# Kernel optimization log

Measured on AMD Instinct MI355X. Metric: run time of the kernel, lower is better.

## Reference

```python
import jax, jax.numpy as jnp
import numpy as np
import math

B, T, D_MODEL, N_HEAD = 2, 2048, 1024, 16
NUM_BUCKETS, MAX_DIST = 32, 128
D_HEAD = D_MODEL // N_HEAD


def _relative_position_bucket(rel_pos, num_buckets=NUM_BUCKETS, max_distance=MAX_DIST):
    # bidirectional=True branch of the torch code
    nb = num_buckets // 2
    buckets = (rel_pos > 0).astype(jnp.int32) * nb
    rel_pos = jnp.abs(rel_pos)
    max_exact = nb // 2
    is_small = rel_pos < max_exact
    # guard log(0); masked out by is_small anyway
    large = max_exact + (
        jnp.log(jnp.maximum(rel_pos, 1).astype(jnp.float32) / max_exact)
        / math.log(max_distance / max_exact) * (nb - max_exact)
    ).astype(jnp.int32)
    large = jnp.minimum(large, nb - 1)
    return buckets + jnp.where(is_small, rel_pos, large)


def compute_bias(rel_bias, q_len, kv_len):
    qp = jnp.arange(q_len, dtype=jnp.int32)[:, None]
    kp = jnp.arange(kv_len, dtype=jnp.int32)[None, :]
    buckets = _relative_position_bucket(kp - qp)          # [Tq, Tkv]
    vals = rel_bias[buckets]                              # [Tq, Tkv, H]
    return jnp.transpose(vals, (2, 0, 1))                 # [H, Tq, Tkv]


def setup_inputs() -> dict:
    key = jax.random.key(0)
    ks = jax.random.split(key, 9)
    inp = {
        'q': jax.random.normal(ks[0], (B, T, D_MODEL), jnp.float32),
        'k': jax.random.normal(ks[1], (B, T, D_MODEL), jnp.float32),
        'v': jax.random.normal(ks[2], (B, T, D_MODEL), jnp.float32),
        'mask': jax.random.randint(ks[3], (B, T, T), 0, 2, jnp.int32),
        'Wq': jax.random.normal(ks[4], (D_MODEL, D_MODEL), jnp.float32) * 0.02,
        'Wk': jax.random.normal(ks[5], (D_MODEL, D_MODEL), jnp.float32) * 0.02,
        'Wv': jax.random.normal(ks[6], (D_MODEL, D_MODEL), jnp.float32) * 0.02,
        'Wfc': jax.random.normal(ks[7], (D_MODEL, D_MODEL), jnp.float32) * 0.02,
        'rel_bias': jax.random.normal(ks[8], (NUM_BUCKETS, N_HEAD), jnp.float32) * 0.02,
    }
    return inp


def reference(q, k, v, mask, Wq, Wk, Wv, Wfc, rel_bias):
    b, tq, _ = q.shape
    tkv = k.shape[1]
    qh = (q @ Wq).reshape(b, tq, N_HEAD, D_HEAD)
    kh = (k @ Wk).reshape(b, tkv, N_HEAD, D_HEAD)
    vh = (v @ Wv).reshape(b, tkv, N_HEAD, D_HEAD)
    attn = jnp.einsum('blhd,bthd->bhlt', qh, kh) / np.sqrt(D_HEAD).astype(np.float32)
    position_bias = compute_bias(rel_bias, tq, tkv)       # [H, Tq, Tkv]
    attn = attn + position_bias[None]                     # broadcast over batch
    attn = jnp.where(mask[:, None] == 0, -1e9, attn)
    attn = jax.nn.softmax(attn, axis=-1)                  # dropout: eval mode (identity)
    out = jnp.einsum('bhlt,bthd->blhd', attn, vh).reshape(b, tq, D_MODEL)
    out = out @ Wfc
    return out, position_bias[:, None]                    # bias returned as [H,1,Tq,Tkv] like torch
```

## Files before the change

kernel.cpp:

```cpp
#include <hip/hip_runtime.h>
#include <math.h>

#define TT 2048
#define BB 2
#define HH 16
#define DMODEL 1024
#define NREL 4095

typedef __attribute__((ext_vector_type(8)))  _Float16 half8;
typedef __attribute__((ext_vector_type(4)))  _Float16 half4;
typedef __attribute__((ext_vector_type(16))) float    f32x16;
typedef __attribute__((ext_vector_type(4)))  int      int4v;

#define EXP2F(x) __builtin_amdgcn_exp2f(x)

__device__ __forceinline__ f32x16 zero16() {
    f32x16 v;
#pragma unroll
    for (int i = 0; i < 16; ++i) v[i] = 0.f;
    return v;
}

__device__ __forceinline__ unsigned pkh(float a, float b) {
    union { _Float16 h[2]; unsigned u; } x;
    x.h[0] = (_Float16)a; x.h[1] = (_Float16)b;
    return x.u;
}

__device__ __forceinline__ void gload16(const void* g, void* l) {
    __builtin_amdgcn_global_load_lds(
        (const __attribute__((address_space(1))) void*)g,
        (__attribute__((address_space(3))) void*)l, 16, 0, 0);
}

__device__ __forceinline__ int rel_bucket(int rel) {
    int base = rel > 0 ? 16 : 0;
    int r = rel < 0 ? -rel : rel;
    int lb;
    if (r < 8)       lb = r;
    else if (r < 12) lb = 8;
    else if (r < 16) lb = 9;
    else if (r < 23) lb = 10;
    else if (r < 32) lb = 11;
    else if (r < 46) lb = 12;
    else if (r < 64) lb = 13;
    else if (r < 91) lb = 14;
    else             lb = 15;
    return base + lb;
}

__global__ __launch_bounds__(256) void prep_kernel(
    const int* __restrict__ mask,
    const float* __restrict__ W0, const float* __restrict__ W1,
    const float* __restrict__ W2, const float* __restrict__ W3,
    const float* __restrict__ rel_bias,
    _Float16* __restrict__ WT,
    float* __restrict__ btable, unsigned* __restrict__ mb)
{
    __shared__ float t[64][65];
    int bid = blockIdx.x, tid = threadIdx.x;
    if (bid < 256) {
        int idx = bid * 256 + tid;
        if (idx < HH * NREL) {
            int h = idx / NREL, ri = idx % NREL;
            btable[idx] = rel_bias[rel_bucket(ri - (TT - 1)) * HH + h];
        }
    } else if (bid < 1280) {
        int zz = (bid - 256) >> 8, inner = (bid - 256) & 255;
        const float* src = zz == 0 ? W0 : zz == 1 ? W1 : zz == 2 ? W2 : W3;
        _Float16* dst = WT + (size_t)zz * DMODEL * DMODEL;
        int k0 = (inner >> 4) * 64, n0 = (inner & 15) * 64;
        int r = tid >> 4, c4 = (tid & 15) * 4;
#pragma unroll
        for (int i = 0; i < 4; ++i) {
            float4 vv = *(const float4*)(src + (size_t)(k0 + r + 16 * i) * DMODEL + n0 + c4);
            t[r + 16 * i][c4] = vv.x; t[r + 16 * i][c4 + 1] = vv.y;
            t[r + 16 * i][c4 + 2] = vv.z; t[r + 16 * i][c4 + 3] = vv.w;
        }
        __syncthreads();
        int rn = tid >> 2, ck = (tid & 3) * 16;
        half8 h0, h1;
#pragma unroll
        for (int j = 0; j < 8; ++j) h0[j] = (_Float16)t[ck + j][rn];
#pragma unroll
        for (int j = 0; j < 8; ++j) h1[j] = (_Float16)t[ck + 8 + j][rn];
        *(half8*)(dst + (size_t)(n0 + rn) * DMODEL + k0 + ck) = h0;
        *(half8*)(dst + (size_t)(n0 + rn) * DMODEL + k0 + ck + 8) = h1;
    } else {
        int g = (bid - 1280) * 256 + tid;
        int vv = mask[g];
        unsigned long long bal = __ballot(vv != 0);
        if ((g & 63) == 0) {
            int word = g >> 5;
            mb[word]     = (unsigned)bal;
            mb[word + 1] = (unsigned)(bal >> 32);
        }
    }
}

__global__ __launch_bounds__(256) void gemm_proj3(
    const float* __restrict__ qf32, const float* __restrict__ kf32,
    const float* __restrict__ vf32, const _Float16* __restrict__ WT,
    _Float16* __restrict__ qhf, _Float16* __restrict__ khf,
    _Float16* __restrict__ vtf, int zbase)
{
    __shared__ __align__(16) char lds[65536];
    int z = zbase + blockIdx.z;
    const float* A = z == 0 ? qf32 : z == 1 ? kf32 : vf32;
    const _Float16* Bt = WT + (size_t)z * DMODEL * DMODEL;
    int bm = blockIdx.x * 128, bn = blockIdx.y * 128;
    int tid = threadIdx.x;
    int wv = tid >> 6, lane = tid & 63, hi = lane >> 5;
    int lo = lane & 31;
    int wr = wv >> 1, wc = wv & 1;
    int srow = wv * 32 + (lane >> 3);
    int scol = (lane & 7) * 8;
    const float*    Abase = A  + (size_t)(bm + srow) * DMODEL + scol;
    const _Float16* Bbase = Bt + (size_t)(bn + srow) * DMODEL + scol;
    int awoff = wv * 4096 + (lane >> 3) * 128 + (lane & 7) * 16;

    f32x16 acc[2][2];
    acc[0][0] = zero16(); acc[0][1] = zero16();
    acc[1][0] = zero16(); acc[1][1] = zero16();

    float4 ra[8];
    auto loadA = [&](int kt) {
#pragma unroll
        for (int t = 0; t < 4; ++t) {
            ra[2 * t]     = *(const float4*)(Abase + (size_t)t * 8 * DMODEL + kt * 64);
            ra[2 * t + 1] = *(const float4*)(Abase + (size_t)t * 8 * DMODEL + kt * 64 + 4);
        }
    };
    auto gloadB = [&](int buf, int kt) {
#pragma unroll
        for (int t = 0; t < 4; ++t)
            gload16(Bbase + (size_t)t * 8 * DMODEL + kt * 64, lds + buf + 16384 + wv * 4096 + t * 1024);
    };
    auto writeA = [&](int buf) {
#pragma unroll
        for (int t = 0; t < 4; ++t) {
            float4 v0 = ra[2 * t], v1 = ra[2 * t + 1];
            half8 h = {(_Float16)v0.x, (_Float16)v0.y, (_Float16)v0.z, (_Float16)v0.w,
                       (_Float16)v1.x, (_Float16)v1.y, (_Float16)v1.z, (_Float16)v1.w};
            *(half8*)(lds + buf + awoff + t * 1024) = h;
        }
    };
    auto compute = [&](int buf) {
#pragma unroll
        for (int kk = 0; kk < 4; ++kk) {
            int cs = 2 * kk + hi;
            half8 a[2], b[2];
#pragma unroll
            for (int i = 0; i < 2; ++i) {
                a[i] = *(const half8*)(lds + buf + (wr * 64 + i * 32 + lo) * 128 + cs * 16);
                b[i] = *(const half8*)(lds + buf + 16384 + (wc * 64 + i * 32 + lo) * 128 + cs * 16);
            }
            acc[0][0] = __builtin_amdgcn_mfma_f32_32x32x16_f16(a[0], b[0], acc[0][0], 0, 0, 0);
            acc[0][1] = __builtin_amdgcn_mfma_f32_32x32x16_f16(a[0], b[1], acc[0][1], 0, 0, 0);
            acc[1][0] = __builtin_amdgcn_mfma_f32_32x32x16_f16(a[1], b[0], acc[1][0], 0, 0, 0);
            acc[1][1] = __builtin_amdgcn_mfma_f32_32x32x16_f16(a[1], b[1], acc[1][1], 0, 0, 0);
        }
    };

    loadA(0); gloadB(0, 0); writeA(0);
    __syncthreads();
    for (int kt = 0; kt < 16; kt += 2) {
        loadA(kt + 1); gloadB(32768, kt + 1);
        compute(0);
        writeA(32768);
        __syncthreads();
        if (kt + 2 < 16) { loadA(kt + 2); gloadB(0, kt + 2); }
        compute(32768);
        if (kt + 2 < 16) writeA(0);
        __syncthreads();
    }

    if (z < 2) {
        _Float16* C = z == 0 ? qhf : khf;
#pragma unroll
        for (int j = 0; j < 2; ++j) {
            int n = bn + wc * 64 + j * 32 + lo;
            int h = n >> 6, d = n & 63;
#pragma unroll
            for (int i = 0; i < 2; ++i) {
                int mb2 = bm + wr * 64 + i * 32 + 4 * hi;
#pragma unroll
                for (int r = 0; r < 16; ++r) {
                    int m = mb2 + (r & 3) + 8 * (r >> 2);
                    int b = m >> 11, t = m & (TT - 1);
                    C[((size_t)(b * HH + h) * TT + t) * 64 + d] = (_Float16)acc[i][j][r];
                }
            }
        }
    } else {
#pragma unroll
        for (int j = 0; j < 2; ++j) {
            int n = bn + wc * 64 + j * 32 + lo;
            int h = n >> 6, d = n & 63;
#pragma unroll
            for (int i = 0; i < 2; ++i) {
                int mb2 = bm + wr * 64 + i * 32 + 4 * hi;
                int b = mb2 >> 11, tb = mb2 & (TT - 1);
#pragma unroll
                for (int r4 = 0; r4 < 4; ++r4) {
                    half4 hv = {(_Float16)acc[i][j][4 * r4 + 0], (_Float16)acc[i][j][4 * r4 + 1],
                                (_Float16)acc[i][j][4 * r4 + 2], (_Float16)acc[i][j][4 * r4 + 3]};
                    *(half4*)(vtf + ((size_t)(b * HH + h) * 64 + d) * TT + tb + 8 * r4) = hv;
                }
            }
        }
    }
}

__global__ __launch_bounds__(256) void attn_mfma(
    const _Float16* __restrict__ qh, const _Float16* __restrict__ kh,
    const _Float16* __restrict__ vt, const unsigned* __restrict__ maskbits,
    const float* __restrict__ btable, _Float16* __restrict__ Oout)
{
    __shared__ float bias_lds[4096];
    int bid = blockIdx.x;
    int xcd = bid & 7, j = bid >> 3;
    int qt = j & 15, bh = xcd + 8 * (j >> 4);
    int h = bh & 15, b = bh >> 4;
    int tid = threadIdx.x;
    int wv = tid >> 6, lane = tid & 63, lo = lane & 31, hi = lane >> 5;
    int q0 = qt * 128 + wv * 32;

    {
        const float* bsrc = btable + h * NREL;
#pragma unroll
        for (int i = 0; i < 16; ++i) {
            int idx = i * 256 + tid;
            bias_lds[idx] = bsrc[idx < NREL ? idx : NREL - 1] * 1.44269504f;
        }
    }

    const size_t bhoff = (size_t)(b * HH + h);
    const _Float16* Q = qh + (bhoff * TT + q0) * 64;
    const _Float16* K = kh + bhoff * TT * 64;
    const _Float16* V = vt + bhoff * 64 * TT;

    half8 qf[4];
#pragma unroll
    for (int c = 0; c < 4; ++c)
        qf[c] = *(const half8*)(Q + (size_t)lo * 64 + c * 16 + hi * 8);

    const int bofs = (TT - 1) - (q0 + lo) + 4 * hi;
    const unsigned* mw = maskbits + ((size_t)b * TT + q0 + lo) * 64;
    const float SC = 0.125f * 1.44269504f;

    f32x16 acco0 = zero16(), acco1 = zero16();
    float m = -INFINITY, l = 0.f;

    __syncthreads();

    for (int kt = 0; kt < 16; ++kt) {
        int k0 = kt * 128;
        unsigned wmA0 = mw[4 * kt], wmA1 = mw[4 * kt + 1];
        unsigned wmB0 = mw[4 * kt + 2], wmB1 = mw[4 * kt + 3];

        f32x16 sA0 = zero16(), sA1 = zero16(), sB0 = zero16(), sB1 = zero16();
        {
            half8 kf[4];
#pragma unroll
            for (int c = 0; c < 4; ++c)
                kf[c] = *(const half8*)(K + (size_t)(k0 + lo) * 64 + c * 16 + hi * 8);
            __builtin_amdgcn_s_setprio(1);
#pragma unroll
            for (int c = 0; c < 4; ++c)
                sA0 = __builtin_amdgcn_mfma_f32_32x32x16_f16(kf[c], qf[c], sA0, 0, 0, 0);
            __builtin_amdgcn_s_setprio(0);
#pragma unroll
            for (int c = 0; c < 4; ++c)
                kf[c] = *(const half8*)(K + (size_t)(k0 + 32 + lo) * 64 + c * 16 + hi * 8);
            __builtin_amdgcn_s_setprio(1);
#pragma unroll
            for (int c = 0; c < 4; ++c)
                sA1 = __builtin_amdgcn_mfma_f32_32x32x16_f16(kf[c], qf[c], sA1, 0, 0, 0);
            __builtin_amdgcn_s_setprio(0);
#pragma unroll
            for (int c = 0; c < 4; ++c)
                kf[c] = *(const half8*)(K + (size_t)(k0 + 64 + lo) * 64 + c * 16 + hi * 8);
            __builtin_amdgcn_s_setprio(1);
#pragma unroll
            for (int c = 0; c < 4; ++c)
                sB0 = __builtin_amdgcn_mfma_f32_32x32x16_f16(kf[c], qf[c], sB0, 0, 0, 0);
            __builtin_amdgcn_s_setprio(0);
#pragma unroll
            for (int c = 0; c < 4; ++c)
                kf[c] = *(const half8*)(K + (size_t)(k0 + 96 + lo) * 64 + c * 16 + hi * 8);
            __builtin_amdgcn_s_setprio(1);
#pragma unroll
            for (int c = 0; c < 4; ++c)
                sB1 = __builtin_amdgcn_mfma_f32_32x32x16_f16(kf[c], qf[c], sB1, 0, 0, 0);
            __builtin_amdgcn_s_setprio(0);
        }

        unsigned wsA0 = wmA0 >> (hi * 4), wsA1 = wmA1 >> (hi * 4);
        unsigned wsB0 = wmB0 >> (hi * 4), wsB1 = wmB1 >> (hi * 4);
        int bbase = bofs + k0;
#pragma unroll
        for (int r = 0; r < 16; ++r) {
            int sh = (r & 3) + 8 * (r >> 2);
            float a0 = fmaf(sA0[r], SC, bias_lds[bbase + sh]);
            float a1 = fmaf(sA1[r], SC, bias_lds[bbase + sh + 32]);
            float b0 = fmaf(sB0[r], SC, bias_lds[bbase + sh + 64]);
            float b1 = fmaf(sB1[r], SC, bias_lds[bbase + sh + 96]);
            sA0[r] = ((wsA0 >> sh) & 1) ? a0 : -1e9f;
            sA1[r] = ((wsA1 >> sh) & 1) ? a1 : -1e9f;
            sB0[r] = ((wsB0 >> sh) & 1) ? b0 : -1e9f;
            sB1[r] = ((wsB1 >> sh) & 1) ? b1 : -1e9f;
        }

        float tr[8];
#pragma unroll
        for (int r = 0; r < 8; ++r) {
            float x0 = fmaxf(fmaxf(sA0[r], sA0[r + 8]), fmaxf(sA1[r], sA1[r + 8]));
            float x1 = fmaxf(fmaxf(sB0[r], sB0[r + 8]), fmaxf(sB1[r], sB1[r + 8]));
            tr[r] = fmaxf(x0, x1);
        }
#pragma unroll
        for (int r = 0; r < 4; ++r) tr[r] = fmaxf(tr[r], tr[r + 4]);
        float tm = fmaxf(fmaxf(tr[0], tr[1]), fmaxf(tr[2], tr[3]));
        tm = fmaxf(tm, __shfl_xor(tm, 32));
        float mnew = fmaxf(m, tm);
        float corr = EXP2F(m - mnew);
        m = mnew;

#pragma unroll
        for (int r = 0; r < 16; ++r) sA0[r] = EXP2F(sA0[r] - m);
#pragma unroll
        for (int r = 0; r < 16; ++r) sA1[r] = EXP2F(sA1[r] - m);
#pragma unroll
        for (int r = 0; r < 16; ++r) sB0[r] = EXP2F(sB0[r] - m);
#pragma unroll
        for (int r = 0; r < 16; ++r) sB1[r] = EXP2F(sB1[r] - m);
#pragma unroll
        for (int r = 0; r < 8; ++r)
            tr[r] = ((sA0[r] + sA0[r + 8]) + (sA1[r] + sA1[r + 8]))
                  + ((sB0[r] + sB0[r + 8]) + (sB1[r] + sB1[r + 8]));
#pragma unroll
        for (int r = 0; r < 4; ++r) tr[r] += tr[r + 4];
        float rs = (tr[0] + tr[1]) + (tr[2] + tr[3]);
        rs += __shfl_xor(rs, 32);
        l = l * corr + rs;
#pragma unroll
        for (int r = 0; r < 16; ++r) { acco0[r] *= corr; acco1[r] *= corr; }

        half8 pbA[4], pbB[4];
#pragma unroll
        for (int g = 0; g < 2; ++g)
#pragma unroll
            for (int hc = 0; hc < 2; ++hc) {
                int r0 = hc * 8;
                float p0 = g ? sA1[r0 + 0] : sA0[r0 + 0];
                float p1 = g ? sA1[r0 + 1] : sA0[r0 + 1];
                float p2 = g ? sA1[r0 + 2] : sA0[r0 + 2];
                float p3 = g ? sA1[r0 + 3] : sA0[r0 + 3];
                float p4 = g ? sA1[r0 + 4] : sA0[r0 + 4];
                float p5 = g ? sA1[r0 + 5] : sA0[r0 + 5];
                float p6 = g ? sA1[r0 + 6] : sA0[r0 + 6];
                float p7 = g ? sA1[r0 + 7] : sA0[r0 + 7];
                unsigned w0 = pkh(p0, p1);
                unsigned w2 = pkh(p4, p5);
                asm("v_permlane32_swap_b32 %0, %1" : "+v"(w0), "+v"(w2));
                unsigned w1 = pkh(p2, p3);
                unsigned w3 = pkh(p6, p7);
                asm("v_permlane32_swap_b32 %0, %1" : "+v"(w1), "+v"(w3));
                union { int4v i; half8 hf; } cv;
                cv.i = (int4v){(int)w0, (int)w1, (int)w2, (int)w3};
                pbA[2 * g + hc] = cv.hf;
            }
#pragma unroll
        for (int g = 0; g < 2; ++g)
#pragma unroll
            for (int hc = 0; hc < 2; ++hc) {
                int r0 = hc * 8;
                float p0 = g ? sB1[r0 + 0] : sB0[r0 + 0];
                float p1 = g ? sB1[r0 + 1] : sB0[r0 + 1];
                float p2 = g ? sB1[r0 + 2] : sB0[r0 + 2];
                float p3 = g ? sB1[r0 + 3] : sB0[r0 + 3];
                float p4 = g ? sB1[r0 + 4] : sB0[r0 + 4];
                float p5 = g ? sB1[r0 + 5] : sB0[r0 + 5];
                float p6 = g ? sB1[r0 + 6] : sB0[r0 + 6];
                float p7 = g ? sB1[r0 + 7] : sB0[r0 + 7];
                unsigned w0 = pkh(p0, p1);
                unsigned w2 = pkh(p4, p5);
                asm("v_permlane32_swap_b32 %0, %1" : "+v"(w0), "+v"(w2));
                unsigned w1 = pkh(p2, p3);
                unsigned w3 = pkh(p6, p7);
                asm("v_permlane32_swap_b32 %0, %1" : "+v"(w1), "+v"(w3));
                union { int4v i; half8 hf; } cv;
                cv.i = (int4v){(int)w0, (int)w1, (int)w2, (int)w3};
                pbB[2 * g + hc] = cv.hf;
            }

        {
            half8 vf[4];
#pragma unroll
            for (int c = 0; c < 4; ++c)
                vf[c] = *(const half8*)(V + (size_t)lo * TT + k0 + c * 16 + hi * 8);
            __builtin_amdgcn_s_setprio(1);
#pragma unroll
            for (int c = 0; c < 4; ++c)
                acco0 = __builtin_amdgcn_mfma_f32_32x32x16_f16(vf[c], pbA[c], acco0, 0, 0, 0);
            __builtin_amdgcn_s_setprio(0);
#pragma unroll
            for (int c = 0; c < 4; ++c)
                vf[c] = *(const half8*)(V + (size_t)lo * TT + k0 + 64 + c * 16 + hi * 8);
            __builtin_amdgcn_s_setprio(1);
#pragma unroll
            for (int c = 0; c < 4; ++c)
                acco0 = __builtin_amdgcn_mfma_f32_32x32x16_f16(vf[c], pbB[c], acco0, 0, 0, 0);
            __builtin_amdgcn_s_setprio(0);
#pragma unroll
            for (int c = 0; c < 4; ++c)
                vf[c] = *(const half8*)(V + (size_t)(32 + lo) * TT + k0 + c * 16 + hi * 8);
            __builtin_amdgcn_s_setprio(1);
#pragma unroll
            for (int c = 0; c < 4; ++c)
                acco1 = __builtin_amdgcn_mfma_f32_32x32x16_f16(vf[c], pbA[c], acco1, 0, 0, 0);
            __builtin_amdgcn_s_setprio(0);
#pragma unroll
            for (int c = 0; c < 4; ++c)
                vf[c] = *(const half8*)(V + (size_t)(32 + lo) * TT + k0 + 64 + c * 16 + hi * 8);
            __builtin_amdgcn_s_setprio(1);
#pragma unroll
            for (int c = 0; c < 4; ++c)
                acco1 = __builtin_amdgcn_mfma_f32_32x32x16_f16(vf[c], pbB[c], acco1, 0, 0, 0);
            __builtin_amdgcn_s_setprio(0);
        }
    }

    float inv = 1.f / l;
    _Float16* op = Oout + (bhoff * TT + q0 + lo) * 64;
#pragma unroll
    for (int r4 = 0; r4 < 4; ++r4) {
        int d0 = 8 * r4 + 4 * hi;
        half4 h0 = {(_Float16)(acco0[4 * r4 + 0] * inv), (_Float16)(acco0[4 * r4 + 1] * inv),
                    (_Float16)(acco0[4 * r4 + 2] * inv), (_Float16)(acco0[4 * r4 + 3] * inv)};
        *(half4*)(op + d0) = h0;
        half4 h1 = {(_Float16)(acco1[4 * r4 + 0] * inv), (_Float16)(acco1[4 * r4 + 1] * inv),
                    (_Float16)(acco1[4 * r4 + 2] * inv), (_Float16)(acco1[4 * r4 + 3] * inv)};
        *(half4*)(op + d0 + 32) = h1;
    }
}

__global__ __launch_bounds__(256) void fc_bias_kernel(
    const _Float16* __restrict__ O, const _Float16* __restrict__ Bt,
    float* __restrict__ out0, const float* __restrict__ btable,
    float* __restrict__ out1)
{
    __shared__ __align__(16) char lds[65536];
    int bid = blockIdx.x, tid = threadIdx.x;
    if (bid >= 256) {
        const int n4 = HH * TT * TT / 4, stride = 2048 * 256;
        for (int i4 = (bid - 256) * 256 + tid; i4 < n4; i4 += stride) {
            int i = i4 * 4;
            int kk = i & (TT - 1);
            int qq = (i >> 11) & (TT - 1);
            int hh2 = i >> 22;
            const float* btp = btable + hh2 * NREL + (kk - qq + (TT - 1));
            float4 vv = make_float4(btp[0], btp[1], btp[2], btp[3]);
            reinterpret_cast<float4*>(out1)[i4] = vv;
        }
        return;
    }
    int bm = (bid & 31) * 128, bn = (bid >> 5) * 128;
    int wv = tid >> 6, lane = tid & 63, lo = lane & 31, hi = lane >> 5;
    int wr = wv >> 1, wc = wv & 1;
    int srow = wv * 32 + (lane >> 3);
    int scol = (lane & 7) * 8;
    int bb = bm >> 11, tbase = bm & (TT - 1);
    const _Float16* Abase = O + ((size_t)(bb * HH) * TT + tbase + srow) * 64 + scol;
    const _Float16* Bbase = Bt + (size_t)(bn + srow) * DMODEL + scol;

    f32x16 acc[2][2];
    acc[0][0] = zero16(); acc[0][1] = zero16();
    acc[1][0] = zero16(); acc[1][1] = zero16();

    auto stage = [&](int buf, int kt) {
#pragma unroll
        for (int t = 0; t < 4; ++t) {
            gload16(Abase + (size_t)kt * TT * 64 + (size_t)t * 8 * 64, lds + buf + wv * 4096 + t * 1024);
            gload16(Bbase + (size_t)t * 8 * DMODEL + kt * 64, lds + buf + 16384 + wv * 4096 + t * 1024);
        }
    };
    auto compute = [&](int buf) {
#pragma unroll
        for (int kk = 0; kk < 4; ++kk) {
            int cs = 2 * kk + hi;
            half8 a[2], b[2];
#pragma unroll
            for (int i = 0; i < 2; ++i) {
                a[i] = *(const half8*)(lds + buf + (wr * 64 + i * 32 + lo) * 128 + cs * 16);
                b[i] = *(const half8*)(lds + buf + 16384 + (wc * 64 + i * 32 + lo) * 128 + cs * 16);
            }
            acc[0][0] = __builtin_amdgcn_mfma_f32_32x32x16_f16(a[0], b[0], acc[0][0], 0, 0, 0);
            acc[0][1] = __builtin_amdgcn_mfma_f32_32x32x16_f16(a[0], b[1], acc[0][1], 0, 0, 0);
            acc[1][0] = __builtin_amdgcn_mfma_f32_32x32x16_f16(a[1], b[0], acc[1][0], 0, 0, 0);
            acc[1][1] = __builtin_amdgcn_mfma_f32_32x32x16_f16(a[1], b[1], acc[1][1], 0, 0, 0);
        }
    };

    stage(0, 0);
    __syncthreads();
    for (int kt = 0; kt < 16; kt += 2) {
        stage(32768, kt + 1);
        compute(0);
        __syncthreads();
        stage(0, kt + 2 < 16 ? kt + 2 : 15);
        compute(32768);
        __syncthreads();
    }

#pragma unroll
    for (int j = 0; j < 2; ++j) {
        int n = bn + wc * 64 + j * 32 + lo;
#pragma unroll
        for (int i = 0; i < 2; ++i) {
            int mb2 = bm + wr * 64 + i * 32 + 4 * hi;
#pragma unroll
            for (int r = 0; r < 16; ++r) {
                int m = mb2 + (r & 3) + 8 * (r >> 2);
                out0[(size_t)m * DMODEL + n] = acc[i][j][r];
            }
        }
    }
}

extern "C" void kernel_launch(void* const* d_in, const int* in_sizes, int n_in,
                              void* d_out, int out_size, void* d_ws, size_t ws_size,
                              hipStream_t stream) {
    const float* q        = (const float*)d_in[0];
    const float* k        = (const float*)d_in[1];
    const float* v        = (const float*)d_in[2];
    const int*   mask     = (const int*)  d_in[3];
    const float* Wq       = (const float*)d_in[4];
    const float* Wk       = (const float*)d_in[5];
    const float* Wv       = (const float*)d_in[6];
    const float* Wfc      = (const float*)d_in[7];
    const float* rel_bias = (const float*)d_in[8];

    float* out0 = (float*)d_out;
    float* out1 = out0 + (size_t)BB * TT * DMODEL;

    char* w = (char*)d_ws;
    _Float16* O   = (_Float16*)(w);
    _Float16* qhf = (_Float16*)(w + ((size_t)24 << 20));
    _Float16* khf = (_Float16*)(w + ((size_t)32 << 20));
    _Float16* WT  = (_Float16*)(w + ((size_t)40 << 20));
    float*    btable = (float*)(w + ((size_t)48 << 20));
    unsigned* mbits  = (unsigned*)(w + ((size_t)48 << 20) + ((size_t)1 << 19));
    bool big = ws_size >= ((size_t)58 << 20);
    _Float16* vtf = big ? (_Float16*)(w + ((size_t)49 << 20) + ((size_t)1 << 19))
                        : (_Float16*)(w + ((size_t)8 << 20));

    prep_kernel<<<dim3(1280 + BB * TT * TT / 256), dim3(256), 0, stream>>>(
        mask, Wq, Wk, Wv, Wfc, rel_bias, WT, btable, mbits);

    if (big) {
        gemm_proj3<<<dim3(32, 8, 3), dim3(256), 0, stream>>>(q, k, v, WT,
                                                             qhf, khf, vtf, 0);
    } else {
        gemm_proj3<<<dim3(32, 8, 1), dim3(256), 0, stream>>>(q, k, v, WT, qhf, khf, vtf, 0);
        gemm_proj3<<<dim3(32, 8, 1), dim3(256), 0, stream>>>(q, k, v, WT, qhf, khf, vtf, 1);
        gemm_proj3<<<dim3(32, 8, 1), dim3(256), 0, stream>>>(q, k, v, WT, qhf, khf, vtf, 2);
    }

    attn_mfma<<<dim3(BB * HH * 16), dim3(256), 0, stream>>>(
        qhf, khf, vtf, mbits, btable, O);

    fc_bias_kernel<<<dim3(2304), dim3(256), 0, stream>>>(
        O, WT + (size_t)3 * DMODEL * DMODEL, out0, btable, out1);
}
```

Measured before the change: 282.5 us.

## Rewrite attention kernel with 16x16x32 MFMA and 16-row query tiles per wave

Switches the attention kernel from 32x32x16 MFMA tiles over 32 query rows per wave to 16x16x32 MFMA tiles over 16 query rows per wave, with 64-key steps instead of 128. The grid doubles to 1024 blocks so more waves are in flight and register pressure per wave drops. The softmax-to-PV operand reshuffle now takes extra cross-lane shuffles, and each K/V tile is loaded from global memory twice as often per query row.

```diff
diff --git a/kernel.cpp b/kernel.cpp
--- a/kernel.cpp
+++ b/kernel.cpp
@@ -10,6 +10,7 @@
 typedef __attribute__((ext_vector_type(8)))  _Float16 half8;
 typedef __attribute__((ext_vector_type(4)))  _Float16 half4;
 typedef __attribute__((ext_vector_type(16))) float    f32x16;
+typedef __attribute__((ext_vector_type(4)))  float    f32x4;
 typedef __attribute__((ext_vector_type(4)))  int      int4v;
 
 #define EXP2F(x) __builtin_amdgcn_exp2f(x)
@@ -19,6 +20,10 @@
 #pragma unroll
     for (int i = 0; i < 16; ++i) v[i] = 0.f;
     return v;
+}
+
+__device__ __forceinline__ f32x4 zero4() {
+    f32x4 v; v[0] = v[1] = v[2] = v[3] = 0.f; return v;
 }
 
 __device__ __forceinline__ unsigned pkh(float a, float b) {
@@ -212,19 +217,20 @@
     }
 }
 
-__global__ __launch_bounds__(256) void attn_mfma(
+__global__ __launch_bounds__(256) void attn_mfma16(
     const _Float16* __restrict__ qh, const _Float16* __restrict__ kh,
     const _Float16* __restrict__ vt, const unsigned* __restrict__ maskbits,
     const float* __restrict__ btable, _Float16* __restrict__ Oout)
 {
     __shared__ float bias_lds[4096];
     int bid = blockIdx.x;
-    int xcd = bid & 7, j = bid >> 3;
-    int qt = j & 15, bh = xcd + 8 * (j >> 4);
+    int xcd = bid & 7, jj = bid >> 3;
+    int qg = jj & 31, bh = xcd + 8 * (jj >> 5);
     int h = bh & 15, b = bh >> 4;
     int tid = threadIdx.x;
-    int wv = tid >> 6, lane = tid & 63, lo = lane & 31, hi = lane >> 5;
-    int q0 = qt * 128 + wv * 32;
+    int wv = tid >> 6, lane = tid & 63;
+    int col = lane & 15, u = lane >> 4, u4 = u * 4;
+    int q0 = (qg * 4 + wv) * 16;
 
     {
         const float* bsrc = btable + h * NREL;
@@ -240,209 +246,121 @@
     const _Float16* K = kh + bhoff * TT * 64;
     const _Float16* V = vt + bhoff * 64 * TT;
 
-    half8 qf[4];
-#pragma unroll
-    for (int c = 0; c < 4; ++c)
-        qf[c] = *(const half8*)(Q + (size_t)lo * 64 + c * 16 + hi * 8);
-
-    const int bofs = (TT - 1) - (q0 + lo) + 4 * hi;
-    const unsigned* mw = maskbits + ((size_t)b * TT + q0 + lo) * 64;
+    half8 qf[2];
+    qf[0] = *(const half8*)(Q + (size_t)col * 64 + u * 8);
+    qf[1] = *(const half8*)(Q + (size_t)col * 64 + 32 + u * 8);
+
+    const int bofs = (TT - 1) - (q0 + col) + u4;
+    const unsigned* mw = maskbits + ((size_t)b * TT + q0 + col) * 64;
     const float SC = 0.125f * 1.44269504f;
 
-    f32x16 acco0 = zero16(), acco1 = zero16();
+    f32x4 acco[4];
+    acco[0] = zero4(); acco[1] = zero4(); acco[2] = zero4(); acco[3] = zero4();
     float m = -INFINITY, l = 0.f;
 
     __syncthreads();
 
-    for (int kt = 0; kt < 16; ++kt) {
-        int k0 = kt * 128;
-        unsigned wmA0 = mw[4 * kt], wmA1 = mw[4 * kt + 1];
-        unsigned wmB0 = mw[4 * kt + 2], wmB1 = mw[4 * kt + 3];
-
-        f32x16 sA0 = zero16(), sA1 = zero16(), sB0 = zero16(), sB1 = zero16();
+    for (int kt = 0; kt < 32; ++kt) {
+        int k0 = kt * 64;
+        unsigned wm0 = mw[2 * kt], wm1 = mw[2 * kt + 1];
+
+        f32x4 s[4];
         {
-            half8 kf[4];
-#pragma unroll
-            for (int c = 0; c < 4; ++c)
-                kf[c] = *(const half8*)(K + (size_t)(k0 + lo) * 64 + c * 16 + hi * 8);
             __builtin_amdgcn_s_setprio(1);
 #pragma unroll
-            for (int c = 0; c < 4; ++c)
-                sA0 = __builtin_amdgcn_mfma_f32_32x32x16_f16(kf[c], qf[c], sA0, 0, 0, 0);
+            for (int g = 0; g < 4; ++g) {
+                half8 kf0 = *(const half8*)(K + (size_t)(k0 + g * 16 + col) * 64 + u * 8);
+                half8 kf1 = *(const half8*)(K + (size_t)(k0 + g * 16 + col) * 64 + 32 + u * 8);
+                s[g] = __builtin_amdgcn_mfma_f32_16x16x32_f16(kf0, qf[0], zero4(), 0, 0, 0);
+                s[g] = __builtin_amdgcn_mfma_f32_16x16x32_f16(kf1, qf[1], s[g], 0, 0, 0);
+            }
             __builtin_amdgcn_s_setprio(0);
-#pragma unroll
-            for (int c = 0; c < 4; ++c)
-                kf[c] = *(const half8*)(K + (size_t)(k0 + 32 + lo) * 64 + c * 16 + hi * 8);
-            __builtin_amdgcn_s_setprio(1);
-#pragma unroll
-            for (int c = 0; c < 4; ++c)
-                sA1 = __builtin_amdgcn_mfma_f32_32x32x16_f16(kf[c], qf[c], sA1, 0, 0, 0);
-            __builtin_amdgcn_s_setprio(0);
-#pragma unroll
-            for (int c = 0; c < 4; ++c)
-                kf[c] = *(const half8*)(K + (size_t)(k0 + 64 + lo) * 64 + c * 16 + hi * 8);
-            __builtin_amdgcn_s_setprio(1);
-#pragma unroll
-            for (int c = 0; c < 4; ++c)
-                sB0 = __builtin_amdgcn_mfma_f32_32x32x16_f16(kf[c], qf[c], sB0, 0, 0, 0);
-            __builtin_amdgcn_s_setprio(0);
-#pragma unroll
-            for (int c = 0; c < 4; ++c)
-                kf[c] = *(const half8*)(K + (size_t)(k0 + 96 + lo) * 64 + c * 16 + hi * 8);
-            __builtin_amdgcn_s_setprio(1);
-#pragma unroll
-            for (int c = 0; c < 4; ++c)
-                sB1 = __builtin_amdgcn_mfma_f32_32x32x16_f16(kf[c], qf[c], sB1, 0, 0, 0);
-            __builtin_amdgcn_s_setprio(0);
-        }
-
-        unsigned wsA0 = wmA0 >> (hi * 4), wsA1 = wmA1 >> (hi * 4);
-        unsigned wsB0 = wmB0 >> (hi * 4), wsB1 = wmB1 >> (hi * 4);
-        int bbase = bofs + k0;
-#pragma unroll
-        for (int r = 0; r < 16; ++r) {
-            int sh = (r & 3) + 8 * (r >> 2);
-            float a0 = fmaf(sA0[r], SC, bias_lds[bbase + sh]);
-            float a1 = fmaf(sA1[r], SC, bias_lds[bbase + sh + 32]);
-            float b0 = fmaf(sB0[r], SC, bias_lds[bbase + sh + 64]);
-            float b1 = fmaf(sB1[r], SC, bias_lds[bbase + sh + 96]);
-            sA0[r] = ((wsA0 >> sh) & 1) ? a0 : -1e9f;
-            sA1[r] = ((wsA1 >> sh) & 1) ? a1 : -1e9f;
-            sB0[r] = ((wsB0 >> sh) & 1) ? b0 : -1e9f;
-            sB1[r] = ((wsB1 >> sh) & 1) ? b1 : -1e9f;
-        }
-
-        float tr[8];
-#pragma unroll
-        for (int r = 0; r < 8; ++r) {
-            float x0 = fmaxf(fmaxf(sA0[r], sA0[r + 8]), fmaxf(sA1[r], sA1[r + 8]));
-            float x1 = fmaxf(fmaxf(sB0[r], sB0[r + 8]), fmaxf(sB1[r], sB1[r + 8]));
-            tr[r] = fmaxf(x0, x1);
-        }
-#pragma unroll
-        for (int r = 0; r < 4; ++r) tr[r] = fmaxf(tr[r], tr[r + 4]);
-        float tm = fmaxf(fmaxf(tr[0], tr[1]), fmaxf(tr[2], tr[3]));
+        }
+
+#pragma unroll
+        for (int g = 0; g < 4; ++g) {
+            unsigned wsg = ((g < 2) ? wm0 : wm1) >> (((g & 1) * 16) + u4);
+            int bb2 = bofs + k0 + g * 16;
+#pragma unroll
+            for (int r = 0; r < 4; ++r) {
+                float x = fmaf(s[g][r], SC, bias_lds[bb2 + r]);
+                s[g][r] = ((wsg >> r) & 1) ? x : -1e9f;
+            }
+        }
+
+        float tm = s[0][0];
+#pragma unroll
+        for (int g = 0; g < 4; ++g)
+#pragma unroll
+            for (int r = 0; r < 4; ++r) tm = fmaxf(tm, s[g][r]);
+        tm = fmaxf(tm, __shfl_xor(tm, 16));
         tm = fmaxf(tm, __shfl_xor(tm, 32));
         float mnew = fmaxf(m, tm);
         float corr = EXP2F(m - mnew);
         m = mnew;
-
-#pragma unroll
-        for (int r = 0; r < 16; ++r) sA0[r] = EXP2F(sA0[r] - m);
-#pragma unroll
-        for (int r = 0; r < 16; ++r) sA1[r] = EXP2F(sA1[r] - m);
-#pragma unroll
-        for (int r = 0; r < 16; ++r) sB0[r] = EXP2F(sB0[r] - m);
-#pragma unroll
-        for (int r = 0; r < 16; ++r) sB1[r] = EXP2F(sB1[r] - m);
-#pragma unroll
-        for (int r = 0; r < 8; ++r)
-            tr[r] = ((sA0[r] + sA0[r + 8]) + (sA1[r] + sA1[r + 8]))
-                  + ((sB0[r] + sB0[r + 8]) + (sB1[r] + sB1[r + 8]));
-#pragma unroll
-        for (int r = 0; r < 4; ++r) tr[r] += tr[r + 4];
-        float rs = (tr[0] + tr[1]) + (tr[2] + tr[3]);
+#pragma unroll
+        for (int g = 0; g < 4; ++g)
+#pragma unroll
+            for (int r = 0; r < 4; ++r) s[g][r] = EXP2F(s[g][r] - m);
+        float rs = 0.f;
+#pragma unroll
+        for (int g = 0; g < 4; ++g)
+            rs += (s[g][0] + s[g][1]) + (s[g][2] + s[g][3]);
+        rs += __shfl_xor(rs, 16);
         rs += __shfl_xor(rs, 32);
         l = l * corr + rs;
 #pragma unroll
-        for (int r = 0; r < 16; ++r) { acco0[r] *= corr; acco1[r] *= corr; }
-
-        half8 pbA[4], pbB[4];
-#pragma unroll
-        for (int g = 0; g < 2; ++g)
-#pragma unroll
-            for (int hc = 0; hc < 2; ++hc) {
-                int r0 = hc * 8;
-                float p0 = g ? sA1[r0 + 0] : sA0[r0 + 0];
-                float p1 = g ? sA1[r0 + 1] : sA0[r0 + 1];
-                float p2 = g ? sA1[r0 + 2] : sA0[r0 + 2];
-                float p3 = g ? sA1[r0 + 3] : sA0[r0 + 3];
-                float p4 = g ? sA1[r0 + 4] : sA0[r0 + 4];
-                float p5 = g ? sA1[r0 + 5] : sA0[r0 + 5];
-                float p6 = g ? sA1[r0 + 6] : sA0[r0 + 6];
-                float p7 = g ? sA1[r0 + 7] : sA0[r0 + 7];
-                unsigned w0 = pkh(p0, p1);
-                unsigned w2 = pkh(p4, p5);
-                asm("v_permlane32_swap_b32 %0, %1" : "+v"(w0), "+v"(w2));
-                unsigned w1 = pkh(p2, p3);
-                unsigned w3 = pkh(p6, p7);
-                asm("v_permlane32_swap_b32 %0, %1" : "+v"(w1), "+v"(w3));
-                union { int4v i; half8 hf; } cv;
-                cv.i = (int4v){(int)w0, (int)w1, (int)w2, (int)w3};
-                pbA[2 * g + hc] = cv.hf;
-            }
-#pragma unroll
-        for (int g = 0; g < 2; ++g)
-#pragma unroll
-            for (int hc = 0; hc < 2; ++hc) {
-                int r0 = hc * 8;
-                float p0 = g ? sB1[r0 + 0] : sB0[r0 + 0];
-                float p1 = g ? sB1[r0 + 1] : sB0[r0 + 1];
-                float p2 = g ? sB1[r0 + 2] : sB0[r0 + 2];
-                float p3 = g ? sB1[r0 + 3] : sB0[r0 + 3];
-                float p4 = g ? sB1[r0 + 4] : sB0[r0 + 4];
-                float p5 = g ? sB1[r0 + 5] : sB0[r0 + 5];
-                float p6 = g ? sB1[r0 + 6] : sB0[r0 + 6];
-                float p7 = g ? sB1[r0 + 7] : sB0[r0 + 7];
-                unsigned w0 = pkh(p0, p1);
-                unsigned w2 = pkh(p4, p5);
-                asm("v_permlane32_swap_b32 %0, %1" : "+v"(w0), "+v"(w2));
-                unsigned w1 = pkh(p2, p3);
-                unsigned w3 = pkh(p6, p7);
-                asm("v_permlane32_swap_b32 %0, %1" : "+v"(w1), "+v"(w3));
-                union { int4v i; half8 hf; } cv;
-                cv.i = (int4v){(int)w0, (int)w1, (int)w2, (int)w3};
-                pbB[2 * g + hc] = cv.hf;
-            }
+        for (int d = 0; d < 4; ++d)
+#pragma unroll
+            for (int r = 0; r < 4; ++r) acco[d][r] *= corr;
+
+        unsigned wA[4], wB[4];
+#pragma unroll
+        for (int g = 0; g < 4; ++g) {
+            wA[g] = pkh(s[g][0], s[g][1]);
+            wB[g] = pkh(s[g][2], s[g][3]);
+        }
+        bool ue = (u & 1) == 0;
+        half8 pb[2];
+#pragma unroll
+        for (int c = 0; c < 2; ++c) {
+            unsigned X = wA[2 * c], Y = wA[2 * c + 1];
+            asm("v_permlane32_swap_b32 %0, %1" : "+v"(X), "+v"(Y));
+            unsigned Xs = (unsigned)__shfl_xor((int)X, 16);
+            unsigned Ys = (unsigned)__shfl_xor((int)Y, 16);
+            unsigned XB = wB[2 * c], YB = wB[2 * c + 1];
+            asm("v_permlane32_swap_b32 %0, %1" : "+v"(XB), "+v"(YB));
+            unsigned XBs = (unsigned)__shfl_xor((int)XB, 16);
+            unsigned YBs = (unsigned)__shfl_xor((int)YB, 16);
+            unsigned d0 = ue ? X : Ys;
+            unsigned d1 = ue ? XB : YBs;
+            unsigned d2 = ue ? Xs : Y;
+            unsigned d3 = ue ? XBs : YB;
+            union { int4v i; half8 hf; } cv;
+            cv.i = (int4v){(int)d0, (int)d1, (int)d2, (int)d3};
+            pb[c] = cv.hf;
+        }
 
         {
-            half8 vf[4];
-#pragma unroll
-            for (int c = 0; c < 4; ++c)
-                vf[c] = *(const half8*)(V + (size_t)lo * TT + k0 + c * 16 + hi * 8);
             __builtin_amdgcn_s_setprio(1);
 #pragma unroll
-            for (int c = 0; c < 4; ++c)
-                acco0 = __builtin_amdgcn_mfma_f32_32x32x16_f16(vf[c], pbA[c], acco0, 0, 0, 0);
+            for (int d = 0; d < 4; ++d) {
+                half8 vf0 = *(const half8*)(V + (size_t)(d * 16 + col) * TT + k0 + u * 8);
+                half8 vf1 = *(const half8*)(V + (size_t)(d * 16 + col) * TT + k0 + 32 + u * 8);
+                acco[d] = __builtin_amdgcn_mfma_f32_16x16x32_f16(vf0, pb[0], acco[d], 0, 0, 0);
+                acco[d] = __builtin_amdgcn_mfma_f32_16x16x32_f16(vf1, pb[1], acco[d], 0, 0, 0);
+            }
             __builtin_amdgcn_s_setprio(0);
-#pragma unroll
-            for (int c = 0; c < 4; ++c)
-                vf[c] = *(const half8*)(V + (size_t)lo * TT + k0 + 64 + c * 16 + hi * 8);
-            __builtin_amdgcn_s_setprio(1);
-#pragma unroll
-            for (int c = 0; c < 4; ++c)
-                acco0 = __builtin_amdgcn_mfma_f32_32x32x16_f16(vf[c], pbB[c], acco0, 0, 0, 0);
-            __builtin_amdgcn_s_setprio(0);
-#pragma unroll
-            for (int c = 0; c < 4; ++c)
-                vf[c] = *(const half8*)(V + (size_t)(32 + lo) * TT + k0 + c * 16 + hi * 8);
-            __builtin_amdgcn_s_setprio(1);
-#pragma unroll
-            for (int c = 0; c < 4; ++c)
-                acco1 = __builtin_amdgcn_mfma_f32_32x32x16_f16(vf[c], pbA[c], acco1, 0, 0, 0);
-            __builtin_amdgcn_s_setprio(0);
-#pragma unroll
-            for (int c = 0; c < 4; ++c)
-                vf[c] = *(const half8*)(V + (size_t)(32 + lo) * TT + k0 + 64 + c * 16 + hi * 8);
-            __builtin_amdgcn_s_setprio(1);
-#pragma unroll
-            for (int c = 0; c < 4; ++c)
-                acco1 = __builtin_amdgcn_mfma_f32_32x32x16_f16(vf[c], pbB[c], acco1, 0, 0, 0);
-            __builtin_amdgcn_s_setprio(0);
         }
     }
 
     float inv = 1.f / l;
-    _Float16* op = Oout + (bhoff * TT + q0 + lo) * 64;
-#pragma unroll
-    for (int r4 = 0; r4 < 4; ++r4) {
-        int d0 = 8 * r4 + 4 * hi;
-        half4 h0 = {(_Float16)(acco0[4 * r4 + 0] * inv), (_Float16)(acco0[4 * r4 + 1] * inv),
-                    (_Float16)(acco0[4 * r4 + 2] * inv), (_Float16)(acco0[4 * r4 + 3] * inv)};
-        *(half4*)(op + d0) = h0;
-        half4 h1 = {(_Float16)(acco1[4 * r4 + 0] * inv), (_Float16)(acco1[4 * r4 + 1] * inv),
-                    (_Float16)(acco1[4 * r4 + 2] * inv), (_Float16)(acco1[4 * r4 + 3] * inv)};
-        *(half4*)(op + d0 + 32) = h1;
+    _Float16* op = Oout + (bhoff * TT + q0 + col) * 64;
+#pragma unroll
+    for (int d = 0; d < 4; ++d) {
+        half4 hv = {(_Float16)(acco[d][0] * inv), (_Float16)(acco[d][1] * inv),
+                    (_Float16)(acco[d][2] * inv), (_Float16)(acco[d][3] * inv)};
+        *(half4*)(op + d * 16 + u4) = hv;
     }
 }
 
@@ -568,7 +486,7 @@
         gemm_proj3<<<dim3(32, 8, 1), dim3(256), 0, stream>>>(q, k, v, WT, qhf, khf, vtf, 2);
     }
 
-    attn_mfma<<<dim3(BB * HH * 16), dim3(256), 0, stream>>>(
+    attn_mfma16<<<dim3(BB * HH * 32), dim3(256), 0, stream>>>(
         qhf, khf, vtf, mbits, btable, O);
 
     fc_bias_kernel<<<dim3(2304), dim3(256), 0, stream>>>(
```

Measured after the change: 405.6 us. +43.6%, slower.
